# Kernel optimization log

Measured on AMD Instinct MI355X. Metric: run time of the kernel, lower is better.

Reference implementation:

```python
import jax, jax.numpy as jnp
import numpy as np

# ---- model dims (match init_kwargs) ----
B, C, T = 64, 128, 512          # batch, n_channel, n_tokens
H = 256                          # n_hidden
GRID_SIZE = 5
SPLINE_ORDER = 3
N_COEFF = GRID_SIZE + SPLINE_ORDER   # 8 basis functions per input feature
GRID_RANGE = (-1.0, 1.0)
LN_EPS = 1e-5


def make_grid(in_features):
    # efficient-KAN extended knot grid: (in_features, grid_size + 2*order + 1)
    h = (GRID_RANGE[1] - GRID_RANGE[0]) / GRID_SIZE
    g = jnp.arange(-SPLINE_ORDER, GRID_SIZE + SPLINE_ORDER + 1, dtype=jnp.float32) * h + GRID_RANGE[0]
    return jnp.broadcast_to(g, (in_features, g.shape[0]))


def b_splines(x, grid):
    # x: (N, in), grid: (in, G+2k+1) -> (N, in, G+k) via Cox-de Boor recursion
    xg = x[:, :, None]
    bases = ((xg >= grid[:, :-1]) & (xg < grid[:, 1:])).astype(x.dtype)
    for k in range(1, SPLINE_ORDER + 1):
        left = (xg - grid[:, : -(k + 1)]) / (grid[:, k:-1] - grid[:, : -(k + 1)])
        right = (grid[:, k + 1:] - xg) / (grid[:, k + 1:] - grid[:, 1:-k])
        bases = left * bases[:, :, :-1] + right * bases[:, :, 1:]
    return bases


def kan_linear(x, grid, base_w, spline_w, spline_scaler):
    # x: (..., in) -> (..., out). base: silu(x)@W^T, plus spline combination.
    lead = x.shape[:-1]
    x2 = x.reshape(-1, x.shape[-1])
    base_out = jax.nn.silu(x2) @ base_w.T                              # (N, out)
    sw = spline_w * spline_scaler[:, :, None]                          # (out, in, coeff)
    spl_out = jnp.einsum('nic,oic->no', b_splines(x2, grid), sw)       # (N, out)
    return (base_out + spl_out).reshape(*lead, base_w.shape[0])


def setup_inputs() -> dict:
    key = jax.random.key(0)
    ks = jax.random.split(key, 8)
    scale1 = 1.0 / np.sqrt(C)
    scale2 = 1.0 / np.sqrt(H)
    return {
        "U": jax.random.normal(ks[0], (B, C, T), dtype=jnp.float32),
        "ln_w": jnp.ones((T, C), dtype=jnp.float32),
        "ln_b": jnp.zeros((T, C), dtype=jnp.float32),
        "bw1": jax.random.normal(ks[1], (H, C), dtype=jnp.float32) * scale1,
        "sw1": jax.random.normal(ks[2], (H, C, N_COEFF), dtype=jnp.float32) * (0.1 * scale1),
        "ss1": jnp.ones((H, C), dtype=jnp.float32),
        "bw2": jax.random.normal(ks[3], (C, H), dtype=jnp.float32) * scale2,
        "sw2": jax.random.normal(ks[4], (C, H, N_COEFF), dtype=jnp.float32) * (0.1 * scale2),
        "ss2": jnp.ones((C, H), dtype=jnp.float32),
    }


def reference(U, ln_w, ln_b, bw1, sw1, ss1, bw2, sw2, ss2):
    g1 = make_grid(C)
    g2 = make_grid(H)
    z = jnp.transpose(U, (0, 2, 1))                                   # (B, T, C)
    mu = jnp.mean(z, axis=(-2, -1), keepdims=True)
    var = jnp.var(z, axis=(-2, -1), keepdims=True)
    z = (z - mu) * jax.lax.rsqrt(var + LN_EPS) * ln_w + ln_b          # LN over [T, C]
    z = kan_linear(z, g1, bw1, sw1, ss1)                              # (B, T, H)
    z = kan_linear(z, g2, bw2, sw2, ss2)                              # (B, T, C)
    return U + jnp.transpose(z, (0, 2, 1))
```

## Files before the change

### kernel.cpp

```cpp
#include <hip/hip_runtime.h>
#include <math.h>

namespace {

constexpr int Bn = 64;
constexpr int Cn = 128;
constexpr int Tn = 512;
constexpr int Hn = 256;
constexpr int MR = 64;
constexpr int TB = Tn / MR;
constexpr int K1 = Cn * 9;
constexpr int K2 = Hn * 9;
constexpr int FC = 16;
constexpr int KC = 144;
constexpr int KSS = 152;
constexpr int HS = 272;
constexpr int NCH1 = 8;
constexpr int NCH2 = 16;
constexpr float LN_EPS = 1e-5f;

typedef __attribute__((ext_vector_type(8))) short short8;
typedef __attribute__((ext_vector_type(16))) float f32x16;

__device__ __forceinline__ unsigned short f2bf(float f) {
  unsigned int u = __builtin_bit_cast(unsigned int, f);
  u = (u + 0x7fffu + ((u >> 16) & 1u)) >> 16;
  return (unsigned short)u;
}
__device__ __forceinline__ float bf2f(unsigned short u) {
  unsigned int v = (unsigned int)u << 16;
  return __builtin_bit_cast(float, v);
}

__device__ __forceinline__ void emit_act(float z,
                                         unsigned short* __restrict__ rowp,
                                         int feat) {
  const float e = __expf(-z);
  const float sil = z * __builtin_amdgcn_rcpf(1.0f + e);
  rowp[128 + feat] = f2bf(sil);
  const float p = z * 2.5f + 5.5f;
  const float fi = floorf(p);
  const int i = (int)fi;
  if (i >= 0 && i <= 10) {
    const float u = p - fi;
    const float u2 = u * u, u3 = u2 * u, t = 1.0f - u;
    const float w0 = t * t * t * (1.0f / 6.0f);
    const float w1 = (3.0f * u3 - 6.0f * u2 + 4.0f) * (1.0f / 6.0f);
    const float w2 =
        (-3.0f * u3 + 3.0f * u2 + 3.0f * u + 1.0f) * (1.0f / 6.0f);
    const float w3 = u3 * (1.0f / 6.0f);
    if (i >= 3) rowp[(i - 3) * 16 + feat] = f2bf(w0);
    if (i >= 2 && i <= 9) rowp[(i - 2) * 16 + feat] = f2bf(w1);
    if (i >= 1 && i <= 8) rowp[(i - 1) * 16 + feat] = f2bf(w2);
    if (i <= 7) rowp[i * 16 + feat] = f2bf(w3);
  }
}

}

__global__ __launch_bounds__(256) void kan_prep(
    const float* __restrict__ U, const float* __restrict__ bw1,
    const float* __restrict__ sw1, const float* __restrict__ ss1,
    const float* __restrict__ bw2, const float* __restrict__ sw2,
    const float* __restrict__ ss2, unsigned short* __restrict__ W1p,
    unsigned short* __restrict__ W2p, float* __restrict__ stats) {
  __shared__ float red[2][4];
  const int blk = blockIdx.x;
  if (blk < 256) {
    int idx = blk * 256 + threadIdx.x;
    if (idx < Hn * Cn) {
      const int h = idx >> 7, c = idx & 127;
      const float* spw = sw1 + ((size_t)h * Cn + c) * 8;
      const float sc = ss1[h * Cn + c];
      unsigned short* dst = W1p + (size_t)h * K1 + (c >> 4) * KC + (c & 15);
#pragma unroll
      for (int j = 0; j < 8; ++j) dst[j * 16] = f2bf(spw[j] * sc);
      dst[8 * 16] = f2bf(bw1[h * Cn + c]);
    } else {
      idx -= Hn * Cn;
      const int c = idx >> 8, h = idx & 255;
      const float* spw = sw2 + ((size_t)c * Hn + h) * 8;
      const float sc = ss2[c * Hn + h];
      unsigned short* dst = W2p + (size_t)c * K2 + (h >> 4) * KC + (h & 15);
#pragma unroll
      for (int j = 0; j < 8; ++j) dst[j * 16] = f2bf(spw[j] * sc);
      dst[8 * 16] = f2bf(bw2[c * Hn + h]);
    }
  } else {
    const int sblk = blk - 256;
    const int b = sblk >> 2, q = sblk & 3;
    const float4* p =
        (const float4*)(U + (size_t)b * (Cn * Tn) + q * (Cn * Tn / 4));
    float s = 0.f, s2 = 0.f;
#pragma unroll 4
    for (int i = threadIdx.x; i < (Cn * Tn / 4) / 4; i += 256) {
      const float4 v = p[i];
      s += v.x + v.y + v.z + v.w;
      s2 += v.x * v.x + v.y * v.y + v.z * v.z + v.w * v.w;
    }
#pragma unroll
    for (int off = 32; off > 0; off >>= 1) {
      s += __shfl_down(s, off);
      s2 += __shfl_down(s2, off);
    }
    if ((threadIdx.x & 63) == 0) {
      red[0][threadIdx.x >> 6] = s;
      red[1][threadIdx.x >> 6] = s2;
    }
    __syncthreads();
    if (threadIdx.x == 0) {
      stats[b * 8 + q * 2 + 0] = red[0][0] + red[0][1] + red[0][2] + red[0][3];
      stats[b * 8 + q * 2 + 1] = red[1][0] + red[1][1] + red[1][2] + red[1][3];
    }
  }
}

__global__ __launch_bounds__(512, 4) void kan_fused(
    const float* __restrict__ U, const float* __restrict__ ln_w,
    const float* __restrict__ ln_b, const unsigned short* __restrict__ W1p,
    const unsigned short* __restrict__ W2p, const float* __restrict__ stats,
    float* __restrict__ out) {
  __shared__ unsigned short s_buf[2][MR * KSS];
  __shared__ unsigned short s_h1[MR * HS];

  const int tid = threadIdx.x;
  const int b = blockIdx.x >> 3;
  const int t0 = (blockIdx.x & 7) * MR;

  const float* sp = stats + b * 8;
  const float ssum = sp[0] + sp[2] + sp[4] + sp[6];
  const float ssq = sp[1] + sp[3] + sp[5] + sp[7];
  const float inv_n = 1.0f / (float)(Cn * Tn);
  const float mean = ssum * inv_n;
  const float rstd = rsqrtf(ssq * inv_n - mean * mean + LN_EPS);

  const int w = tid >> 6;
  const int l = tid & 63;
  const int ln31 = l & 31;
  const int hl = l >> 5;
  const int feat = tid & 15;
  const int rowq = tid >> 4;

  const short8 zz = {0, 0, 0, 0, 0, 0, 0, 0};

  auto zero_rows = [&](unsigned short* nbuf) {
#pragma unroll
    for (int it = 0; it < 3; ++it) {
      const int i = l + it * 64;
      if (it < 2 || l < 16) {
        const int r8 = i / 18;
        const int off = i - r8 * 18;
        const int row = w * 4 + (r8 & 3) + (r8 >> 2) * 32;
        *(short8*)&nbuf[row * KSS + off * 8] = zz;
      }
    }
  };
  auto act1 = [&](int chunk, unsigned short* nbuf) {
    zero_rows(nbuf);
    const int c = chunk * FC + feat;
#pragma unroll
    for (int pp = 0; pp < 2; ++pp) {
      const int row = rowq + pp * 32;
      const int t = t0 + row;
      const float uv = U[((size_t)b * Cn + c) * Tn + t];
      const float z = (uv - mean) * rstd * ln_w[t * Cn + c] + ln_b[t * Cn + c];
      emit_act(z, nbuf + row * KSS, feat);
    }
  };
  auto act2 = [&](int chunk, unsigned short* nbuf) {
    zero_rows(nbuf);
#pragma unroll
    for (int pp = 0; pp < 2; ++pp) {
      const int row = rowq + pp * 32;
      const float z = bf2f(s_h1[row * HS + chunk * FC + feat]);
      emit_act(z, nbuf + row * KSS, feat);
    }
  };

  const unsigned short* wb1 = W1p + (size_t)(w * 32 + ln31) * K1 + hl * 8;

  short8 breg[9];
#pragma unroll
  for (int ks = 0; ks < 9; ++ks) breg[ks] = *(const short8*)(wb1 + ks * 16);
  act1(0, s_buf[0]);
  __syncthreads();

  f32x16 acc1[2] = {};
  for (int k = 0; k < NCH1; ++k) {
    const unsigned short* cur = s_buf[k & 1];
    if (k < NCH1 - 1) act1(k + 1, s_buf[(k + 1) & 1]);
    const unsigned short* a0p = cur + ln31 * KSS + hl * 8;
#pragma unroll
    for (int ks = 0; ks < 9; ++ks) {
      const short8 a0 = *(const short8*)(a0p + ks * 16);
      const short8 a1 = *(const short8*)(a0p + 32 * KSS + ks * 16);
      const short8 bc = breg[ks];
      if (k < NCH1 - 1)
        breg[ks] = *(const short8*)(wb1 + (k + 1) * KC + ks * 16);
      acc1[0] =
          __builtin_amdgcn_mfma_f32_32x32x16_bf16(a0, bc, acc1[0], 0, 0, 0);
      acc1[1] =
          __builtin_amdgcn_mfma_f32_32x32x16_bf16(a1, bc, acc1[1], 0, 0, 0);
    }
    __syncthreads();
  }

  const int mg2 = w >> 2;
  const int ng2 = w & 3;
  const unsigned short* wb2 = W2p + (size_t)(ng2 * 32 + ln31) * K2 + hl * 8;
#pragma unroll
  for (int ks = 0; ks < 9; ++ks) breg[ks] = *(const short8*)(wb2 + ks * 16);

#pragma unroll
  for (int q = 0; q < 2; ++q)
#pragma unroll
    for (int reg = 0; reg < 16; ++reg) {
      const int row = q * 32 + 4 * hl + (reg & 3) + 8 * (reg >> 2);
      s_h1[row * HS + w * 32 + ln31] = f2bf(acc1[q][reg]);
    }
  __syncthreads();
  act2(0, s_buf[0]);
  __syncthreads();

  f32x16 acc2 = {};
  const int arow2 = mg2 * 32 + ln31;
  for (int k = 0; k < NCH2; ++k) {
    const unsigned short* cur = s_buf[k & 1];
    if (k < NCH2 - 1) act2(k + 1, s_buf[(k + 1) & 1]);
    const unsigned short* ap = cur + arow2 * KSS + hl * 8;
#pragma unroll
    for (int ks = 0; ks < 9; ++ks) {
      const short8 a = *(const short8*)(ap + ks * 16);
      const short8 bc = breg[ks];
      if (k < NCH2 - 1)
        breg[ks] = *(const short8*)(wb2 + (k + 1) * KC + ks * 16);
      acc2 = __builtin_amdgcn_mfma_f32_32x32x16_bf16(a, bc, acc2, 0, 0, 0);
    }
    __syncthreads();
  }

  const int c = ng2 * 32 + ln31;
#pragma unroll
  for (int g = 0; g < 4; ++g) {
    const int tbase = t0 + mg2 * 32 + 4 * hl + 8 * g;
    const size_t base = ((size_t)b * Cn + c) * Tn + tbase;
    const float4 uin = *(const float4*)(U + base);
    float4 o;
    o.x = uin.x + acc2[g * 4 + 0];
    o.y = uin.y + acc2[g * 4 + 1];
    o.z = uin.z + acc2[g * 4 + 2];
    o.w = uin.w + acc2[g * 4 + 3];
    *(float4*)(out + base) = o;
  }
}

extern "C" void kernel_launch(void* const* d_in, const int* in_sizes, int n_in,
                              void* d_out, int out_size, void* d_ws,
                              size_t ws_size, hipStream_t stream) {
  const float* U = (const float*)d_in[0];
  const float* ln_w = (const float*)d_in[1];
  const float* ln_b = (const float*)d_in[2];
  const float* bw1 = (const float*)d_in[3];
  const float* sw1 = (const float*)d_in[4];
  const float* ss1 = (const float*)d_in[5];
  const float* bw2 = (const float*)d_in[6];
  const float* sw2 = (const float*)d_in[7];
  const float* ss2 = (const float*)d_in[8];
  float* out = (float*)d_out;

  float* stats = (float*)d_ws;
  unsigned short* W1p = (unsigned short*)((char*)d_ws + 4096);
  unsigned short* W2p = W1p + (size_t)Hn * K1;

  kan_prep<<<512, 256, 0, stream>>>(U, bw1, sw1, ss1, bw2, sw2, ss2, W1p, W2p,
                                    stats);
  kan_fused<<<Bn * TB, 512, 0, stream>>>(U, ln_w, ln_b, W1p, W2p, stats, out);
}
```

Before: 122.1 us.

## Halve row tile, warp-specialize layer-2 producers and MFMA consumers, pre-transpose LN params

The row tile drops from 64 to 32, which doubles the block count. In layer 2, half the waves now compute the spline and SiLU activations while the other half run the MFMAs at raised priority, so producers and consumers overlap. Layer 1 gets explicit double-buffered B registers, and its global loads are issued before the MFMAs. The LayerNorm weight and bias are pre-transposed to bf16 in the prep kernel so the main kernel reads them coalesced. The spline store becomes branchless by writing out-of-range values to a dummy padding slot. The risks are lower MFMA utilization per block with only 4 consumer waves, weight reloads across twice as many blocks, and bf16 rounding of the LN parameters.

```diff
diff --git a/kernel.cpp b/kernel.cpp
--- a/kernel.cpp
+++ b/kernel.cpp
@@ -3,20 +3,16 @@
 
 namespace {
 
-constexpr int Bn = 64;
-constexpr int Cn = 128;
-constexpr int Tn = 512;
-constexpr int Hn = 256;
-constexpr int MR = 64;
+constexpr int Bn = 64, Cn = 128, Tn = 512, Hn = 256;
+constexpr int MR = 32;
 constexpr int TB = Tn / MR;
 constexpr int K1 = Cn * 9;
 constexpr int K2 = Hn * 9;
 constexpr int FC = 16;
 constexpr int KC = 144;
 constexpr int KSS = 152;
-constexpr int HS = 272;
-constexpr int NCH1 = 8;
-constexpr int NCH2 = 16;
+constexpr int HS = 274;
+constexpr int NCH1 = 8, NCH2 = 16;
 constexpr float LN_EPS = 1e-5f;
 
 typedef __attribute__((ext_vector_type(8))) short short8;
@@ -32,38 +28,39 @@
   return __builtin_bit_cast(float, v);
 }
 
-__device__ __forceinline__ void emit_act(float z,
-                                         unsigned short* __restrict__ rowp,
-                                         int feat) {
+__device__ __forceinline__ void act_store(float z,
+                                          unsigned short* __restrict__ rowp,
+                                          int feat) {
   const float e = __expf(-z);
-  const float sil = z * __builtin_amdgcn_rcpf(1.0f + e);
-  rowp[128 + feat] = f2bf(sil);
+  rowp[128 + feat] = f2bf(z * __builtin_amdgcn_rcpf(1.0f + e));
   const float p = z * 2.5f + 5.5f;
   const float fi = floorf(p);
-  const int i = (int)fi;
-  if (i >= 0 && i <= 10) {
-    const float u = p - fi;
-    const float u2 = u * u, u3 = u2 * u, t = 1.0f - u;
-    const float w0 = t * t * t * (1.0f / 6.0f);
-    const float w1 = (3.0f * u3 - 6.0f * u2 + 4.0f) * (1.0f / 6.0f);
-    const float w2 =
-        (-3.0f * u3 + 3.0f * u2 + 3.0f * u + 1.0f) * (1.0f / 6.0f);
-    const float w3 = u3 * (1.0f / 6.0f);
-    if (i >= 3) rowp[(i - 3) * 16 + feat] = f2bf(w0);
-    if (i >= 2 && i <= 9) rowp[(i - 2) * 16 + feat] = f2bf(w1);
-    if (i >= 1 && i <= 8) rowp[(i - 1) * 16 + feat] = f2bf(w2);
-    if (i <= 7) rowp[i * 16 + feat] = f2bf(w3);
+  const int ib = (int)fi - 3;
+  const float u = p - fi;
+  const float u2 = u * u, u3 = u2 * u, tt = 1.0f - u;
+  const float wv0 = tt * tt * tt * (1.0f / 6.0f);
+  const float wv1 = (3.0f * u3 - 6.0f * u2 + 4.0f) * (1.0f / 6.0f);
+  const float wv2 = (-3.0f * u3 + 3.0f * u2 + 3.0f * u + 1.0f) * (1.0f / 6.0f);
+  const float wv3 = u3 * (1.0f / 6.0f);
+  const float wv[4] = {wv0, wv1, wv2, wv3};
+#pragma unroll
+  for (int s = 0; s < 4; ++s) {
+    const int j = ib + s;
+    const int off = (j >= 0 && j <= 7) ? j * 16 + feat : 144 + (feat & 7);
+    rowp[off] = f2bf(wv[s]);
   }
 }
 
 }
 
 __global__ __launch_bounds__(256) void kan_prep(
-    const float* __restrict__ U, const float* __restrict__ bw1,
+    const float* __restrict__ U, const float* __restrict__ ln_w,
+    const float* __restrict__ ln_b, const float* __restrict__ bw1,
     const float* __restrict__ sw1, const float* __restrict__ ss1,
     const float* __restrict__ bw2, const float* __restrict__ sw2,
     const float* __restrict__ ss2, unsigned short* __restrict__ W1p,
-    unsigned short* __restrict__ W2p, float* __restrict__ stats) {
+    unsigned short* __restrict__ W2p, unsigned short* __restrict__ lnwT,
+    unsigned short* __restrict__ lnbT, float* __restrict__ stats) {
   __shared__ float red[2][4];
   const int blk = blockIdx.x;
   if (blk < 256) {
@@ -86,7 +83,7 @@
       for (int j = 0; j < 8; ++j) dst[j * 16] = f2bf(spw[j] * sc);
       dst[8 * 16] = f2bf(bw2[c * Hn + h]);
     }
-  } else {
+  } else if (blk < 512) {
     const int sblk = blk - 256;
     const int b = sblk >> 2, q = sblk & 3;
     const float4* p =
@@ -112,20 +109,32 @@
       stats[b * 8 + q * 2 + 0] = red[0][0] + red[0][1] + red[0][2] + red[0][3];
       stats[b * 8 + q * 2 + 1] = red[1][0] + red[1][1] + red[1][2] + red[1][3];
     }
+  } else {
+    const int bb = blk - 512;
+    const float* src = (bb < 64) ? ln_w : ln_b;
+    unsigned short* dst = (bb < 64) ? lnwT : lnbT;
+    const int base = (bb & 63) * 1024;
+#pragma unroll
+    for (int e2 = 0; e2 < 4; ++e2) {
+      const int i = base + (int)threadIdx.x + e2 * 256;
+      const int c = i >> 9, t = i & 511;
+      dst[i] = f2bf(src[t * Cn + c]);
+    }
   }
 }
 
 __global__ __launch_bounds__(512, 4) void kan_fused(
-    const float* __restrict__ U, const float* __restrict__ ln_w,
-    const float* __restrict__ ln_b, const unsigned short* __restrict__ W1p,
+    const float* __restrict__ U, const unsigned short* __restrict__ lnwT,
+    const unsigned short* __restrict__ lnbT,
+    const unsigned short* __restrict__ W1p,
     const unsigned short* __restrict__ W2p, const float* __restrict__ stats,
     float* __restrict__ out) {
   __shared__ unsigned short s_buf[2][MR * KSS];
   __shared__ unsigned short s_h1[MR * HS];
 
   const int tid = threadIdx.x;
-  const int b = blockIdx.x >> 3;
-  const int t0 = (blockIdx.x & 7) * MR;
+  const int b = blockIdx.x >> 4;
+  const int t0 = (blockIdx.x & 15) * MR;
 
   const float* sp = stats + b * 8;
   const float ssum = sp[0] + sp[2] + sp[4] + sp[6];
@@ -134,123 +143,151 @@
   const float mean = ssum * inv_n;
   const float rstd = rsqrtf(ssq * inv_n - mean * mean + LN_EPS);
 
-  const int w = tid >> 6;
-  const int l = tid & 63;
-  const int ln31 = l & 31;
-  const int hl = l >> 5;
-  const int feat = tid & 15;
-  const int rowq = tid >> 4;
-
-  const short8 zz = {0, 0, 0, 0, 0, 0, 0, 0};
-
-  auto zero_rows = [&](unsigned short* nbuf) {
-#pragma unroll
-    for (int it = 0; it < 3; ++it) {
-      const int i = l + it * 64;
-      if (it < 2 || l < 16) {
-        const int r8 = i / 18;
-        const int off = i - r8 * 18;
-        const int row = w * 4 + (r8 & 3) + (r8 >> 2) * 32;
-        *(short8*)&nbuf[row * KSS + off * 8] = zz;
-      }
-    }
-  };
-  auto act1 = [&](int chunk, unsigned short* nbuf) {
-    zero_rows(nbuf);
-    const int c = chunk * FC + feat;
+  const int w = tid >> 6, l = tid & 63;
+  const int ln31 = l & 31, hl = l >> 5;
+  const int a_feat = tid >> 5;
+  const int a_row = tid & 31;
+
+  auto zero1 = [&](unsigned short* nbuf) {
+    unsigned int* zb = (unsigned int*)nbuf;
+#pragma unroll
+    for (int it = 0; it < 4; ++it) {
+      const int e = l + it * 64;
+      zb[(e & 31) * (KSS / 2) + (e >> 5) * 8 + w] = 0u;
+    }
+  };
+  auto zero2 = [&](unsigned short* nbuf) {
+    unsigned int* zb = (unsigned int*)nbuf;
+#pragma unroll
+    for (int it = 0; it < 8; ++it) {
+      const int e = l + it * 64;
+      const int idx = e >> 5;
+      zb[(e & 31) * (KSS / 2) + (idx >> 1) * 8 + 2 * w + (idx & 1)] = 0u;
+    }
+  };
+
+  auto act1_load = [&](int chunk, float& uS, unsigned short& wS,
+                       unsigned short& bS) {
+    const int c = chunk * FC + a_feat;
+    const int t = t0 + a_row;
+    uS = U[((size_t)b * Cn + c) * Tn + t];
+    wS = lnwT[c * Tn + t];
+    bS = lnbT[c * Tn + t];
+  };
+  auto act1_fire = [&](unsigned short* nbuf, float uS, unsigned short wS,
+                       unsigned short bS) {
+    zero1(nbuf);
+    const float z = (uS - mean) * rstd * bf2f(wS) + bf2f(bS);
+    act_store(z, nbuf + a_row * KSS, a_feat);
+  };
+  auto act2_all = [&](int chunk, unsigned short* nbuf) {
+    zero2(nbuf);
+    const int pf = tid >> 4;
 #pragma unroll
     for (int pp = 0; pp < 2; ++pp) {
-      const int row = rowq + pp * 32;
-      const int t = t0 + row;
-      const float uv = U[((size_t)b * Cn + c) * Tn + t];
-      const float z = (uv - mean) * rstd * ln_w[t * Cn + c] + ln_b[t * Cn + c];
-      emit_act(z, nbuf + row * KSS, feat);
-    }
-  };
-  auto act2 = [&](int chunk, unsigned short* nbuf) {
-    zero_rows(nbuf);
-#pragma unroll
-    for (int pp = 0; pp < 2; ++pp) {
-      const int row = rowq + pp * 32;
-      const float z = bf2f(s_h1[row * HS + chunk * FC + feat]);
-      emit_act(z, nbuf + row * KSS, feat);
-    }
-  };
-
+      const int row = (l & 15) + pp * 16;
+      const float z = bf2f(s_h1[row * HS + chunk * FC + pf]);
+      act_store(z, nbuf + row * KSS, pf);
+    }
+  };
+
+  short8 breg0[9], breg1[9];
   const unsigned short* wb1 = W1p + (size_t)(w * 32 + ln31) * K1 + hl * 8;
-
-  short8 breg[9];
-#pragma unroll
-  for (int ks = 0; ks < 9; ++ks) breg[ks] = *(const short8*)(wb1 + ks * 16);
-  act1(0, s_buf[0]);
+#pragma unroll
+  for (int ks = 0; ks < 9; ++ks) breg0[ks] = *(const short8*)(wb1 + ks * 16);
+  {
+    float uS;
+    unsigned short wS, bS;
+    act1_load(0, uS, wS, bS);
+    act1_fire(s_buf[0], uS, wS, bS);
+  }
   __syncthreads();
 
-  f32x16 acc1[2] = {};
-  for (int k = 0; k < NCH1; ++k) {
-    const unsigned short* cur = s_buf[k & 1];
-    if (k < NCH1 - 1) act1(k + 1, s_buf[(k + 1) & 1]);
-    const unsigned short* a0p = cur + ln31 * KSS + hl * 8;
-#pragma unroll
-    for (int ks = 0; ks < 9; ++ks) {
-      const short8 a0 = *(const short8*)(a0p + ks * 16);
-      const short8 a1 = *(const short8*)(a0p + 32 * KSS + ks * 16);
-      const short8 bc = breg[ks];
-      if (k < NCH1 - 1)
-        breg[ks] = *(const short8*)(wb1 + (k + 1) * KC + ks * 16);
-      acc1[0] =
-          __builtin_amdgcn_mfma_f32_32x32x16_bf16(a0, bc, acc1[0], 0, 0, 0);
-      acc1[1] =
-          __builtin_amdgcn_mfma_f32_32x32x16_bf16(a1, bc, acc1[1], 0, 0, 0);
-    }
-    __syncthreads();
-  }
-
-  const int mg2 = w >> 2;
-  const int ng2 = w & 3;
-  const unsigned short* wb2 = W2p + (size_t)(ng2 * 32 + ln31) * K2 + hl * 8;
-#pragma unroll
-  for (int ks = 0; ks < 9; ++ks) breg[ks] = *(const short8*)(wb2 + ks * 16);
-
-#pragma unroll
-  for (int q = 0; q < 2; ++q)
-#pragma unroll
-    for (int reg = 0; reg < 16; ++reg) {
-      const int row = q * 32 + 4 * hl + (reg & 3) + 8 * (reg >> 2);
-      s_h1[row * HS + w * 32 + ln31] = f2bf(acc1[q][reg]);
-    }
-  __syncthreads();
-  act2(0, s_buf[0]);
-  __syncthreads();
-
-  f32x16 acc2 = {};
-  const int arow2 = mg2 * 32 + ln31;
-  for (int k = 0; k < NCH2; ++k) {
-    const unsigned short* cur = s_buf[k & 1];
-    if (k < NCH2 - 1) act2(k + 1, s_buf[(k + 1) & 1]);
-    const unsigned short* ap = cur + arow2 * KSS + hl * 8;
+  f32x16 acc1 = {};
+  auto l1step = [&](int kk, const unsigned short* CUR, unsigned short* NXT,
+                    short8(&BC)[9], short8(&BN)[9]) {
+    const bool more = kk < NCH1 - 1;
+    float uS = 0.f;
+    unsigned short wS = 0, bS = 0;
+    if (more) {
+#pragma unroll
+      for (int ks = 0; ks < 9; ++ks)
+        BN[ks] = *(const short8*)(wb1 + (kk + 1) * KC + ks * 16);
+      act1_load(kk + 1, uS, wS, bS);
+    }
+    __builtin_amdgcn_sched_barrier(0);
+    const unsigned short* ap = CUR + ln31 * KSS + hl * 8;
 #pragma unroll
     for (int ks = 0; ks < 9; ++ks) {
       const short8 a = *(const short8*)(ap + ks * 16);
-      const short8 bc = breg[ks];
-      if (k < NCH2 - 1)
-        breg[ks] = *(const short8*)(wb2 + (k + 1) * KC + ks * 16);
-      acc2 = __builtin_amdgcn_mfma_f32_32x32x16_bf16(a, bc, acc2, 0, 0, 0);
-    }
+      acc1 = __builtin_amdgcn_mfma_f32_32x32x16_bf16(a, BC[ks], acc1, 0, 0, 0);
+    }
+    if (more) act1_fire(NXT, uS, wS, bS);
     __syncthreads();
-  }
-
-  const int c = ng2 * 32 + ln31;
-#pragma unroll
-  for (int g = 0; g < 4; ++g) {
-    const int tbase = t0 + mg2 * 32 + 4 * hl + 8 * g;
-    const size_t base = ((size_t)b * Cn + c) * Tn + tbase;
-    const float4 uin = *(const float4*)(U + base);
-    float4 o;
-    o.x = uin.x + acc2[g * 4 + 0];
-    o.y = uin.y + acc2[g * 4 + 1];
-    o.z = uin.z + acc2[g * 4 + 2];
-    o.w = uin.w + acc2[g * 4 + 3];
-    *(float4*)(out + base) = o;
+  };
+  for (int k = 0; k < NCH1; k += 2) {
+    l1step(k, s_buf[0], s_buf[1], breg0, breg1);
+    l1step(k + 1, s_buf[1], s_buf[0], breg1, breg0);
+  }
+
+  const unsigned short* wb2 = W2p + (size_t)((w & 3) * 32 + ln31) * K2 + hl * 8;
+  if (w >= 4) {
+#pragma unroll
+    for (int ks = 0; ks < 9; ++ks) breg0[ks] = *(const short8*)(wb2 + ks * 16);
+  }
+#pragma unroll
+  for (int r = 0; r < 16; ++r) {
+    const int row = 4 * hl + (r & 3) + 8 * (r >> 2);
+    s_h1[row * HS + w * 32 + ln31] = f2bf(acc1[r]);
+  }
+  __syncthreads();
+  if (w < 4) act2_all(0, s_buf[0]);
+  __syncthreads();
+
+  f32x16 acc2 = {};
+  auto l2step = [&](int kk, const unsigned short* CUR, unsigned short* NXT,
+                    short8(&BC)[9], short8(&BN)[9]) {
+    const bool more = kk < NCH2 - 1;
+    if (w >= 4) {
+      if (more) {
+#pragma unroll
+        for (int ks = 0; ks < 9; ++ks)
+          BN[ks] = *(const short8*)(wb2 + (kk + 1) * KC + ks * 16);
+      }
+      __builtin_amdgcn_sched_barrier(0);
+      const unsigned short* ap = CUR + ln31 * KSS + hl * 8;
+      __builtin_amdgcn_s_setprio(1);
+#pragma unroll
+      for (int ks = 0; ks < 9; ++ks) {
+        const short8 a = *(const short8*)(ap + ks * 16);
+        acc2 =
+            __builtin_amdgcn_mfma_f32_32x32x16_bf16(a, BC[ks], acc2, 0, 0, 0);
+      }
+      __builtin_amdgcn_s_setprio(0);
+    } else {
+      if (more) act2_all(kk + 1, NXT);
+    }
+    __syncthreads();
+  };
+  for (int k = 0; k < NCH2; k += 2) {
+    l2step(k, s_buf[0], s_buf[1], breg0, breg1);
+    l2step(k + 1, s_buf[1], s_buf[0], breg1, breg0);
+  }
+
+  if (w >= 4) {
+    const int c = (w & 3) * 32 + ln31;
+#pragma unroll
+    for (int g = 0; g < 4; ++g) {
+      const int tb = t0 + 4 * hl + 8 * g;
+      const size_t base = ((size_t)b * Cn + c) * Tn + tb;
+      const float4 uin = *(const float4*)(U + base);
+      float4 o;
+      o.x = uin.x + acc2[g * 4 + 0];
+      o.y = uin.y + acc2[g * 4 + 1];
+      o.z = uin.z + acc2[g * 4 + 2];
+      o.w = uin.w + acc2[g * 4 + 3];
+      *(float4*)(out + base) = o;
+    }
   }
 }
 
@@ -268,11 +305,14 @@
   const float* ss2 = (const float*)d_in[8];
   float* out = (float*)d_out;
 
-  float* stats = (float*)d_ws;
-  unsigned short* W1p = (unsigned short*)((char*)d_ws + 4096);
+  char* ws = (char*)d_ws;
+  float* stats = (float*)ws;
+  unsigned short* lnwT = (unsigned short*)(ws + 4096);
+  unsigned short* lnbT = lnwT + Cn * Tn;
+  unsigned short* W1p = lnbT + Cn * Tn;
   unsigned short* W2p = W1p + (size_t)Hn * K1;
 
-  kan_prep<<<512, 256, 0, stream>>>(U, bw1, sw1, ss1, bw2, sw2, ss2, W1p, W2p,
-                                    stats);
-  kan_fused<<<Bn * TB, 512, 0, stream>>>(U, ln_w, ln_b, W1p, W2p, stats, out);
-}
+  kan_prep<<<640, 256, 0, stream>>>(U, ln_w, ln_b, bw1, sw1, ss1, bw2, sw2,
+                                    ss2, W1p, W2p, lnwT, lnbT, stats);
+  kan_fused<<<Bn * TB, 512, 0, stream>>>(U, lnwT, lnbT, W1p, W2p, stats, out);
+}
```

Result: slower. 151.3 us (+23.9%).
